# Kernel optimization log

Measured on AMD Instinct MI355X. Metric: run time of the kernel, lower is better.

## Reference

```python
import jax, jax.numpy as jnp
import numpy as np

EPS = 1e-6

def _phi(x):
    # elu_feature_map: elu(x) + 1 (positive feature map)
    return jax.nn.elu(x) + 1.0

def setup_inputs() -> dict:
    key = jax.random.key(0)
    ks = jax.random.split(key, 6)
    N, L, S, H, E, D = 4, 2048, 2048, 16, 64, 64
    return {
        "queries1": jax.random.normal(ks[0], (N, L, H, E), jnp.float32),
        "keys1": jax.random.normal(ks[1], (N, S, H, E), jnp.float32),
        "values1": jax.random.normal(ks[2], (N, S, H, D), jnp.float32),
        "queries2": jax.random.normal(ks[3], (N, L, H, E), jnp.float32),
        "keys2": jax.random.normal(ks[4], (N, S, H, E), jnp.float32),
        "values2": jax.random.normal(ks[5], (N, S, H, D), jnp.float32),
        "key_lengths1": jnp.ones((N, S), jnp.float32),
        "key_lengths2": jnp.ones((N, S), jnp.float32),
    }

def _linear_cross(Q, K_other, V_other):
    # Q: (N,L,H,E) featurized queries; K_other: (N,S,H,E) featurized+masked keys
    # KV: (N,H,D,E) ; 'nshd,nshm->nhmd'
    KV = jnp.einsum('nshd,nshm->nhmd', K_other, V_other)
    Ksum = K_other.sum(axis=1)                      # (N,H,E)
    Z = 1.0 / (jnp.einsum('nlhd,nhd->nlh', Q, Ksum) + EPS)
    # 'nlhd,nhmd,nlh->nlhm'
    return jnp.einsum('nlhd,nhmd->nlhm', Q, KV) * Z[..., None]

def reference(queries1, keys1, values1, queries2, keys2, values2,
              key_lengths1, key_lengths2):
    Q1 = _phi(queries1)
    K1 = _phi(keys1) * key_lengths1[:, :, None, None]
    Q2 = _phi(queries2)
    K2 = _phi(keys2) * key_lengths2[:, :, None, None]
    V1 = _linear_cross(Q1, K2, values2)  # stream1 queries attend to stream2 keys/values
    V2 = _linear_cross(Q2, K1, values1)  # stream2 queries attend to stream1 keys/values
    return (V1, V2)
```

## Files before the change

kernel.cpp:

```cpp
#include <hip/hip_runtime.h>

#define NB 4
#define LL 2048
#define SS 2048
#define HH 16
#define EE 64
#define DD 64

#define NHEAD (2*NB*HH)
#define NCHUNK 8
#define KVP   ((size_t)NHEAD*NCHUNK*4096)
#define KVOUT (KVP + (size_t)NHEAD*NCHUNK*64)
#define WSFLOATS (KVOUT + (size_t)NHEAD*4096)

typedef short short8 __attribute__((ext_vector_type(8)));
typedef float floatx4 __attribute__((ext_vector_type(4)));

__device__ inline float phi(float x) { return x > 0.f ? x + 1.f : __expf(x); }

__device__ inline void split_pack(float a, float b, unsigned int &hp, unsigned int &lp) {
    unsigned int h, l;
    asm("v_cvt_pk_bf16_f32 %0, %1, %2" : "=v"(h) : "v"(a), "v"(b));
    const float ra = a - __uint_as_float(h << 16);
    const float rb = b - __uint_as_float(h & 0xFFFF0000u);
    asm("v_cvt_pk_bf16_f32 %0, %1, %2" : "=v"(l) : "v"(ra), "v"(rb));
    hp = h; lp = l;
}

__device__ inline void soft_barrier() {
    asm volatile("s_waitcnt lgkmcnt(0)" ::: "memory");
    __builtin_amdgcn_sched_barrier(0);
    __builtin_amdgcn_s_barrier();
    __builtin_amdgcn_sched_barrier(0);
}

__device__ inline int swz(int row, int col) {
    return ((((col >> 3) ^ ((row >> 2) ^ row)) & 7) << 3) | (col & 7);
}

__global__ __launch_bounds__(256) void kv_kernel(
    const float* __restrict__ k1, const float* __restrict__ v1,
    const float* __restrict__ k2, const float* __restrict__ v2,
    const float* __restrict__ kl1, const float* __restrict__ kl2,
    float* __restrict__ ws)
{
    const int b = blockIdx.x;
    const int chunk = b & 7;
    const int h = (b >> 3) & 15;
    const int n = (b >> 7) & 3;
    const int st = (b >> 9) & 1;
    const float* K  = st ? k1 : k2;
    const float* V  = st ? v1 : v2;
    const float* KL = st ? kl1 : kl2;

    __shared__ __align__(16) unsigned short KtH[64][64];
    __shared__ __align__(16) unsigned short KtL[64][64];
    __shared__ __align__(16) unsigned short VtH[64][64];
    __shared__ __align__(16) unsigned short VtL[64][64];

    const int t = threadIdx.x;
    const int lane = t & 63;
    const int w = t >> 6;
    const int d4 = t & 15;
    const int sp = t >> 4;
    const int c = lane & 15;
    const int q = lane >> 4;

    float ksum[4] = {0.f, 0.f, 0.f, 0.f};
    floatx4 acc[4];
#pragma unroll
    for (int i = 0; i < 4; i++) acc[i] = (floatx4){0.f, 0.f, 0.f, 0.f};

    float4 cur[8]; float curl[4];
    {
        const int sbase = chunk * 256;
#pragma unroll
        for (int i = 0; i < 2; ++i) {
            const int sl = 2 * sp + 32 * i;
            const size_t off = ((size_t)((size_t)n * SS + sbase + sl) * HH + h) * EE + 4 * d4;
            cur[4 * i + 0] = *(const float4*)&K[off];
            cur[4 * i + 1] = *(const float4*)&K[off + HH * EE];
            cur[4 * i + 2] = *(const float4*)&V[off];
            cur[4 * i + 3] = *(const float4*)&V[off + HH * EE];
            curl[2 * i + 0] = KL[(size_t)n * SS + sbase + sl];
            curl[2 * i + 1] = KL[(size_t)n * SS + sbase + sl + 1];
        }
    }

    for (int g = 0; g < 4; ++g) {
        float4 nxt[8]; float nxtl[4];
        if (g < 3) {
            const int sbase = chunk * 256 + (g + 1) * 64;
#pragma unroll
            for (int i = 0; i < 2; ++i) {
                const int sl = 2 * sp + 32 * i;
                const size_t off = ((size_t)((size_t)n * SS + sbase + sl) * HH + h) * EE + 4 * d4;
                nxt[4 * i + 0] = *(const float4*)&K[off];
                nxt[4 * i + 1] = *(const float4*)&K[off + HH * EE];
                nxt[4 * i + 2] = *(const float4*)&V[off];
                nxt[4 * i + 3] = *(const float4*)&V[off + HH * EE];
                nxtl[2 * i + 0] = KL[(size_t)n * SS + sbase + sl];
                nxtl[2 * i + 1] = KL[(size_t)n * SS + sbase + sl + 1];
            }
        }
        if (g) soft_barrier();
#pragma unroll
        for (int i = 0; i < 2; ++i) {
            const int sl = 2 * sp + 32 * i;
            const float4 ka = cur[4 * i + 0], kb = cur[4 * i + 1];
            const float4 va = cur[4 * i + 2], vb = cur[4 * i + 3];
            const float l0 = curl[2 * i + 0], l1 = curl[2 * i + 1];
            const float a0 = phi(ka.x) * l0, a1 = phi(ka.y) * l0;
            const float a2 = phi(ka.z) * l0, a3 = phi(ka.w) * l0;
            const float b0 = phi(kb.x) * l1, b1 = phi(kb.y) * l1;
            const float b2 = phi(kb.z) * l1, b3 = phi(kb.w) * l1;
            ksum[0] += a0 + b0; ksum[1] += a1 + b1;
            ksum[2] += a2 + b2; ksum[3] += a3 + b3;
            unsigned int hp, lp;
            const int r0 = 4 * d4;
            const int s0 = swz(r0 + 0, sl), s1 = swz(r0 + 1, sl);
            const int s2 = swz(r0 + 2, sl), s3 = swz(r0 + 3, sl);
            split_pack(a0, b0, hp, lp);
            *(unsigned int*)&KtH[r0 + 0][s0] = hp; *(unsigned int*)&KtL[r0 + 0][s0] = lp;
            split_pack(a1, b1, hp, lp);
            *(unsigned int*)&KtH[r0 + 1][s1] = hp; *(unsigned int*)&KtL[r0 + 1][s1] = lp;
            split_pack(a2, b2, hp, lp);
            *(unsigned int*)&KtH[r0 + 2][s2] = hp; *(unsigned int*)&KtL[r0 + 2][s2] = lp;
            split_pack(a3, b3, hp, lp);
            *(unsigned int*)&KtH[r0 + 3][s3] = hp; *(unsigned int*)&KtL[r0 + 3][s3] = lp;
            split_pack(va.x, vb.x, hp, lp);
            *(unsigned int*)&VtH[r0 + 0][s0] = hp; *(unsigned int*)&VtL[r0 + 0][s0] = lp;
            split_pack(va.y, vb.y, hp, lp);
            *(unsigned int*)&VtH[r0 + 1][s1] = hp; *(unsigned int*)&VtL[r0 + 1][s1] = lp;
            split_pack(va.z, vb.z, hp, lp);
            *(unsigned int*)&VtH[r0 + 2][s2] = hp; *(unsigned int*)&VtL[r0 + 2][s2] = lp;
            split_pack(va.w, vb.w, hp, lp);
            *(unsigned int*)&VtH[r0 + 3][s3] = hp; *(unsigned int*)&VtL[r0 + 3][s3] = lp;
        }
        soft_barrier();
        const int ra = 16 * w + c;
#pragma unroll
        for (int ks = 0; ks < 2; ++ks) {
            const int ca = swz(ra, 32 * ks + 8 * q);
            const short8 aH = *(const short8*)&VtH[ra][ca];
            const short8 aL = *(const short8*)&VtL[ra][ca];
#pragma unroll
            for (int dt = 0; dt < 4; ++dt) {
                const int rb = 16 * dt + c;
                const int cb = swz(rb, 32 * ks + 8 * q);
                const short8 bH = *(const short8*)&KtH[rb][cb];
                const short8 bL = *(const short8*)&KtL[rb][cb];
                acc[dt] = __builtin_amdgcn_mfma_f32_16x16x32_bf16(aH, bH, acc[dt], 0, 0, 0);
                acc[dt] = __builtin_amdgcn_mfma_f32_16x16x32_bf16(aH, bL, acc[dt], 0, 0, 0);
                acc[dt] = __builtin_amdgcn_mfma_f32_16x16x32_bf16(aL, bH, acc[dt], 0, 0, 0);
            }
        }
        if (g < 3) {
#pragma unroll
            for (int i = 0; i < 8; ++i) cur[i] = nxt[i];
#pragma unroll
            for (int i = 0; i < 4; ++i) curl[i] = nxtl[i];
        }
    }

    const int head = (st * NB + n) * HH + h;
    const size_t kvbase = ((size_t)head * NCHUNK + chunk) * 4096;
#pragma unroll
    for (int dt = 0; dt < 4; ++dt)
#pragma unroll
        for (int r = 0; r < 4; ++r)
            ws[kvbase + (size_t)(16 * w + 4 * q + r) * 64 + 16 * dt + c] = acc[dt][r];

    float (*scr)[64] = (float(*)[64])VtL;
    soft_barrier();
    scr[sp][4 * d4 + 0] = ksum[0];
    scr[sp][4 * d4 + 1] = ksum[1];
    scr[sp][4 * d4 + 2] = ksum[2];
    scr[sp][4 * d4 + 3] = ksum[3];
    soft_barrier();
    if (t < 64) {
        float s = 0.f;
#pragma unroll
        for (int i = 0; i < 16; ++i) s += scr[i][t];
        ws[KVP + ((size_t)head * NCHUNK + chunk) * 64 + t] = s;
    }
}

__global__ __launch_bounds__(256) void reduce_kernel(float* __restrict__ ws)
{
    const int bq = blockIdx.x;
    const int head = bq >> 2;
    const int qt = bq & 3;
    const int t = threadIdx.x;
    const size_t base = (size_t)head * (NCHUNK * 4096);
    const int m = qt * 16 + (t >> 4);
    const int d0 = (t & 15) * 4;
    const size_t eo = (size_t)m * 64 + d0;

    float4 s = *(const float4*)&ws[base + eo];
#pragma unroll
    for (int ch = 1; ch < NCHUNK; ++ch) {
        const float4 p = *(const float4*)&ws[base + (size_t)ch * 4096 + eo];
        s.x += p.x; s.y += p.y; s.z += p.z; s.w += p.w;
    }

    const int fm = ((m >> 2) ^ m) & 7;
    unsigned int* W = (unsigned int*)&ws[KVOUT + (size_t)head * 4096];
    const int bp = ((((d0 >> 3) ^ fm) & 7) << 2) + ((d0 & 4) >> 1);
    unsigned int hp, lp;
    split_pack(s.x, s.y, hp, lp);
    W[m * 32 + bp]     = hp;  W[2048 + m * 32 + bp]     = lp;
    split_pack(s.z, s.w, hp, lp);
    W[m * 32 + bp + 1] = hp;  W[2048 + m * 32 + bp + 1] = lp;

    if (qt == 0 && t < 64) {
        float ks = 0.f;
#pragma unroll
        for (int ch = 0; ch < NCHUNK; ++ch)
            ks += ws[KVP + ((size_t)head * NCHUNK + ch) * 64 + t];
        ws[KVP + (size_t)head * NCHUNK * 64 + t] = ks;
    }
}

static __device__ __forceinline__ float lt_body(
    const float4 qa0, const float4 qb0, const float4 qa1, const float4 qb1,
    const float* Ksp,
    const unsigned short (*BH)[64], const unsigned short (*BL)[64],
    const int c, const int q, floatx4* acc)
{
    float z = 0.f;
#pragma unroll
    for (int ks = 0; ks < 2; ++ks) {
        const float4 qa = ks ? qa1 : qa0;
        const float4 qb = ks ? qb1 : qb0;
        const int co = 32 * ks + 8 * q;
        const float p[8] = {phi(qa.x), phi(qa.y), phi(qa.z), phi(qa.w),
                            phi(qb.x), phi(qb.y), phi(qb.z), phi(qb.w)};
        z += p[0] * Ksp[co + 0] + p[1] * Ksp[co + 1]
           + p[2] * Ksp[co + 2] + p[3] * Ksp[co + 3]
           + p[4] * Ksp[co + 4] + p[5] * Ksp[co + 5]
           + p[6] * Ksp[co + 6] + p[7] * Ksp[co + 7];
        short8 aH, aL;
        unsigned int* ah = (unsigned int*)&aH;
        unsigned int* al = (unsigned int*)&aL;
#pragma unroll
        for (int j = 0; j < 4; ++j) {
            unsigned int hp, lp;
            split_pack(p[2 * j], p[2 * j + 1], hp, lp);
            ah[j] = hp; al[j] = lp;
        }
#pragma unroll
        for (int mt = 0; mt < 4; ++mt) {
            const int rb = 16 * mt + c;
            const int cb = swz(rb, co);
            const short8 bH = *(const short8*)&BH[rb][cb];
            const short8 bL = *(const short8*)&BL[rb][cb];
            acc[mt] = __builtin_amdgcn_mfma_f32_16x16x32_bf16(aH, bH, acc[mt], 0, 0, 0);
            acc[mt] = __builtin_amdgcn_mfma_f32_16x16x32_bf16(aH, bL, acc[mt], 0, 0, 0);
            acc[mt] = __builtin_amdgcn_mfma_f32_16x16x32_bf16(aL, bH, acc[mt], 0, 0, 0);
        }
    }
    return z;
}

__global__ __launch_bounds__(256) void out_kernel(
    const float* __restrict__ q1, const float* __restrict__ q2,
    const float* __restrict__ ws, float* __restrict__ out)
{
    const int b = blockIdx.x;
    const int lc = b & 15;
    const int h = (b >> 4) & 15;
    const int n = (b >> 8) & 3;
    const int st = (b >> 10) & 1;
    const float* Q = st ? q2 : q1;
    float* O = out + (size_t)st * ((size_t)NB * LL * HH * DD);

    __shared__ __align__(16) unsigned short BtH[64][64];
    __shared__ __align__(16) unsigned short BtL[64][64];
    __shared__ float Ks[64];

    const int t = threadIdx.x;
    const int lane = t & 63;
    const int w = t >> 6;
    const int c = lane & 15;
    const int q = lane >> 4;
    const int head = (st * NB + n) * HH + h;
    const int lbase = lc * 128;

    const float* qr0 = &Q[((size_t)((size_t)n * LL + lbase + 32 * w + c) * HH + h) * EE];
    const int d0q = 8 * q;
    const float4 p00 = *(const float4*)&qr0[d0q];
    const float4 p01 = *(const float4*)&qr0[d0q + 4];
    const float4 p02 = *(const float4*)&qr0[d0q + 32];
    const float4 p03 = *(const float4*)&qr0[d0q + 36];
    const float* qr1 = qr0 + (size_t)16 * HH * EE;
    const float4 p10 = *(const float4*)&qr1[d0q];
    const float4 p11 = *(const float4*)&qr1[d0q + 4];
    const float4 p12 = *(const float4*)&qr1[d0q + 32];
    const float4 p13 = *(const float4*)&qr1[d0q + 36];

    {
        const uint4* src = (const uint4*)(ws + KVOUT + (size_t)head * 4096);
        uint4* dstH = (uint4*)&BtH[0][0];
        uint4* dstL = (uint4*)&BtL[0][0];
        dstH[t]       = src[t];
        dstH[t + 256] = src[t + 256];
        dstL[t]       = src[512 + t];
        dstL[t + 256] = src[768 + t];
    }
    if (t < 64) Ks[t] = ws[KVP + (size_t)head * NCHUNK * 64 + t];
    soft_barrier();

    floatx4 acc[8];
#pragma unroll
    for (int i = 0; i < 8; ++i) acc[i] = (floatx4){0.f, 0.f, 0.f, 0.f};

    float z0 = lt_body(p00, p01, p02, p03, Ks, BtH, BtL, c, q, acc);
    float z1 = lt_body(p10, p11, p12, p13, Ks, BtH, BtL, c, q, acc + 4);

    z0 += __shfl_xor(z0, 16); z0 += __shfl_xor(z0, 32);
    z1 += __shfl_xor(z1, 16); z1 += __shfl_xor(z1, 32);
    const float zi0 = 1.f / (z0 + 1e-6f);
    const float zi1 = 1.f / (z1 + 1e-6f);

#pragma unroll
    for (int lt = 0; lt < 2; ++lt) {
        const float zi = lt ? zi1 : zi0;
#pragma unroll
        for (int r = 0; r < 4; ++r) {
            const float zz = __shfl(zi, 4 * q + r);
            const int ll = 32 * w + 16 * lt + 4 * q + r;
            const size_t ro = ((size_t)((size_t)n * LL + lbase + ll) * HH + h) * DD;
#pragma unroll
            for (int mt = 0; mt < 4; ++mt)
                O[ro + 16 * mt + c] = acc[4 * lt + mt][r] * zz;
        }
    }
}

extern "C" void kernel_launch(void* const* d_in, const int* in_sizes, int n_in,
                              void* d_out, int out_size, void* d_ws, size_t ws_size,
                              hipStream_t stream) {
    const float* q1  = (const float*)d_in[0];
    const float* k1  = (const float*)d_in[1];
    const float* v1  = (const float*)d_in[2];
    const float* q2  = (const float*)d_in[3];
    const float* k2  = (const float*)d_in[4];
    const float* v2  = (const float*)d_in[5];
    const float* kl1 = (const float*)d_in[6];
    const float* kl2 = (const float*)d_in[7];
    float* ws = (float*)d_ws;
    float* out = (float*)d_out;

    kv_kernel<<<dim3(1024), dim3(256), 0, stream>>>(k1, v1, k2, v2, kl1, kl2, ws);
    reduce_kernel<<<dim3(512), dim3(256), 0, stream>>>(ws);
    out_kernel<<<dim3(2048), dim3(256), 0, stream>>>(q1, q2, ws, out);
}
```

Baseline: 241.6 us.

## Use software bf16 rounding, plain syncthreads, and remap out-kernel block order

```diff
diff --git a/kernel.cpp b/kernel.cpp
--- a/kernel.cpp
+++ b/kernel.cpp
@@ -18,13 +18,16 @@
 
 __device__ inline float phi(float x) { return x > 0.f ? x + 1.f : __expf(x); }
 
+__device__ inline unsigned int f2bf(float f) {
+    unsigned int x = __float_as_uint(f);
+    return (x + 0x7FFFu + ((x >> 16) & 1u)) >> 16;
+}
 __device__ inline void split_pack(float a, float b, unsigned int &hp, unsigned int &lp) {
-    unsigned int h, l;
-    asm("v_cvt_pk_bf16_f32 %0, %1, %2" : "=v"(h) : "v"(a), "v"(b));
-    const float ra = a - __uint_as_float(h << 16);
-    const float rb = b - __uint_as_float(h & 0xFFFF0000u);
-    asm("v_cvt_pk_bf16_f32 %0, %1, %2" : "=v"(l) : "v"(ra), "v"(rb));
-    hp = h; lp = l;
+    const unsigned int ha = f2bf(a), hb = f2bf(b);
+    const float ra = a - __uint_as_float(ha << 16);
+    const float rb = b - __uint_as_float(hb << 16);
+    hp = (ha & 0xFFFFu) | (hb << 16);
+    lp = (f2bf(ra) & 0xFFFFu) | (f2bf(rb) << 16);
 }
 
 __device__ inline void soft_barrier() {
@@ -103,7 +106,7 @@
                 nxtl[2 * i + 1] = KL[(size_t)n * SS + sbase + sl + 1];
             }
         }
-        if (g) soft_barrier();
+        if (g) __syncthreads();
 #pragma unroll
         for (int i = 0; i < 2; ++i) {
             const int sl = 2 * sp + 32 * i;
@@ -137,7 +140,7 @@
             split_pack(va.w, vb.w, hp, lp);
             *(unsigned int*)&VtH[r0 + 3][s3] = hp; *(unsigned int*)&VtL[r0 + 3][s3] = lp;
         }
-        soft_barrier();
+        __syncthreads();
         const int ra = 16 * w + c;
 #pragma unroll
         for (int ks = 0; ks < 2; ++ks) {
@@ -172,12 +175,12 @@
             ws[kvbase + (size_t)(16 * w + 4 * q + r) * 64 + 16 * dt + c] = acc[dt][r];
 
     float (*scr)[64] = (float(*)[64])VtL;
-    soft_barrier();
+    __syncthreads();
     scr[sp][4 * d4 + 0] = ksum[0];
     scr[sp][4 * d4 + 1] = ksum[1];
     scr[sp][4 * d4 + 2] = ksum[2];
     scr[sp][4 * d4 + 3] = ksum[3];
-    soft_barrier();
+    __syncthreads();
     if (t < 64) {
         float s = 0.f;
 #pragma unroll
@@ -241,13 +244,11 @@
            + p[4] * Ksp[co + 4] + p[5] * Ksp[co + 5]
            + p[6] * Ksp[co + 6] + p[7] * Ksp[co + 7];
         short8 aH, aL;
-        unsigned int* ah = (unsigned int*)&aH;
-        unsigned int* al = (unsigned int*)&aL;
-#pragma unroll
-        for (int j = 0; j < 4; ++j) {
-            unsigned int hp, lp;
-            split_pack(p[2 * j], p[2 * j + 1], hp, lp);
-            ah[j] = hp; al[j] = lp;
+#pragma unroll
+        for (int j = 0; j < 8; ++j) {
+            const unsigned int hb = f2bf(p[j]);
+            aH[j] = (short)hb;
+            aL[j] = (short)f2bf(p[j] - __uint_as_float(hb << 16));
         }
 #pragma unroll
         for (int mt = 0; mt < 4; ++mt) {
@@ -268,9 +269,9 @@
     const float* __restrict__ ws, float* __restrict__ out)
 {
     const int b = blockIdx.x;
-    const int lc = b & 15;
-    const int h = (b >> 4) & 15;
-    const int n = (b >> 8) & 3;
+    const int h  = b & 15;
+    const int lc = (b >> 4) & 15;
+    const int n  = (b >> 8) & 3;
     const int st = (b >> 10) & 1;
     const float* Q = st ? q2 : q1;
     float* O = out + (size_t)st * ((size_t)NB * LL * HH * DD);
```

Result: no change. 243.6 us (+0.8%).
